# Performance work log

Measured on AMD Instinct MI355X. Metric: run time of the kernel, lower is better.

The kernel has to match this reference:

```python
import jax, jax.numpy as jnp
import numpy as np

KH = KW = 3  # kernel spatial size is hard-coded to 3 in the original layer


def _tdiv2(x):
    # matches tf.cast(x / 2, tf.int32): true-divide by 2, truncate toward zero
    return jnp.trunc(x * 0.5)


def setup_inputs() -> dict:
    key = jax.random.key(0)
    k1, k2, k3 = jax.random.split(key, 3)
    B, H, W, C, F = 4, 32, 32, 64, 128
    # integer-valued tensors stored as float32 (bit-serial math needs integer weights)
    inputs = jax.random.randint(k1, (B, H, W, C), 0, 16).astype(jnp.float32)
    kernel = jax.random.randint(k2, (KH, KW, C, F), -8, 8).astype(jnp.float32)
    bias = jax.random.randint(k3, (F,), -4, 4).astype(jnp.float32)
    return {"inputs": inputs, "kernel": kernel, "bias": bias, "bits": 4}


def reference(inputs, kernel, bias, bits):
    # Bit-serial conv2d, padding='same' (pad=1), activation='relu'.
    # Per (kernel position, input element, output channel) the original computes
    #   acc <- trunc((acc + x * (w mod 2) * sign(w_orig)) / 2); w <- trunc(w / 2)
    # for `bits` iterations, then sums over channels/kernel window.
    B, H, W, C = inputs.shape
    F = kernel.shape[-1]
    x = jnp.pad(inputs, ((0, 0), (1, 1), (1, 1), (0, 0)))  # 'same' padding, pad=1
    out = jnp.zeros((B, H, W, F), inputs.dtype)
    for i in range(KH):
        for j in range(KW):
            patch = x[:, i:i + H, j:j + W, :][..., None]   # [B,H,W,C,1]
            w = kernel[i, j]                               # [C,F]
            s = jnp.sign(w)                                # sign of ORIGINAL weight, fixed
            acc = jnp.zeros((B, H, W, C, F), inputs.dtype)
            ww = w
            for _ in range(bits):
                acc = _tdiv2(acc + patch * (jnp.mod(ww, 2.0) * s))
                ww = _tdiv2(ww)
            out = out + acc.sum(axis=3)                    # sum over C; kernel window summed by loop
    return jax.nn.relu(out + bias)
```

## Files before the change

### kernel.cpp

```cpp
#include <hip/hip_runtime.h>
#include <stdint.h>


typedef short s16x2 __attribute__((ext_vector_type(2)));

#define NWPK 36864
#define XOFF 36864
#define NXPK 147968

__global__ __launch_bounds__(256) void prep_all(const float* __restrict__ kern,
                                                const float* __restrict__ input,
                                                uint32_t* __restrict__ ws) {
    int bid = blockIdx.x, tid = threadIdx.x;
    if (bid < 144) {
        int t  = bid * 256 + tid;
        int u  = t & 3;
        int f  = (t >> 2) & 127;
        int cq = (t >> 9) & 3;
        int gk = t >> 11;
        int g  = gk & 1;
        int ki = gk >> 1;
        int c  = cq * 16 + g * 8 + u * 2;
        int wlo = (int)kern[(ki * 64 + c    ) * 128 + f];
        int whi = (int)kern[(ki * 64 + c + 1) * 128 + f];
        ws[t] = (uint32_t)(uint16_t)(int16_t)wlo |
                ((uint32_t)(uint16_t)(int16_t)whi << 16);
    } else {
        int t = (bid - 144) * 256 + tid;
        if (t >= NXPK) return;
        int c2    = t & 31;
        int rest  = t >> 5;
        int wp    = rest % 34;
        int rest2 = rest / 34;
        int hp    = rest2 % 34;
        int b     = rest2 / 34;
        int v = 0;
        if (hp >= 1 && hp <= 32 && wp >= 1 && wp <= 32) {
            const float* p = &input[(((b * 32) + hp - 1) * 32 + (wp - 1)) * 64 + c2 * 2];
            v = (int)p[0] | ((int)p[1] << 16);
        }
        ws[XOFF + t] = (uint32_t)v;
    }
}

__global__ __launch_bounds__(512, 4) void conv_main(const uint32_t* __restrict__ ws,
                                                    const float* __restrict__ bias,
                                                    float* __restrict__ out) {
    const uint32_t* xpk = ws + XOFF;

    int bid = blockIdx.x;
    int wq  = bid & 7;
    int h   = (bid >> 3) & 31;
    int b   = bid >> 8;
    int tid = threadIdx.x;
    int f   = tid & 127;
    int cq  = tid >> 7;
    int w0  = wq * 4;

    __shared__ uint32_t xl[3 * 6 * 32];
    __shared__ int prt[4 * 4 * 128];

    if (tid < 576) {
        int c2  = tid & 31;
        int rc  = tid >> 5;
        int col = rc % 6;
        int r   = rc / 6;
        xl[tid] = xpk[((b * 34 + h + r) * 34 + (w0 + col)) * 32 + c2];
    } else {
        int k   = tid - 512;
    }
    if (tid < 64) {
        int k   = tid + 512;
        int c2  = k & 31;
        int rc  = k >> 5;
        int col = rc % 6;
        int r   = rc / 6;
        xl[k] = xpk[((b * 34 + h + r) * 34 + (w0 + col)) * 32 + c2];
    }

    int4 wv[18];
    const int4* wp = (const int4*)ws;
    #pragma unroll
    for (int i = 0; i < 18; ++i) wv[i] = wp[i * 512 + tid];

    __syncthreads();

    s16x2 acc0 = {0,0}, acc1 = {0,0}, acc2 = {0,0}, acc3 = {0,0};

    #pragma unroll
    for (int ki = 0; ki < 9; ++ki) {
        const int row = ki / 3, jj = ki % 3;
        #pragma unroll
        for (int g = 0; g < 2; ++g) {
            const int4 w4 = wv[ki * 2 + g];
            const uint32_t* xrow = xl + (row * 6 + jj) * 32 + cq * 8 + g * 4;
            int4 xv0 = *(const int4*)(xrow);
            int4 xv1 = *(const int4*)(xrow + 32);
            int4 xv2 = *(const int4*)(xrow + 64);
            int4 xv3 = *(const int4*)(xrow + 96);
            #pragma unroll
            for (int u = 0; u < 4; ++u) {
                s16x2 w2 = __builtin_bit_cast(s16x2, (&w4.x)[u]);
                s16x2 A  = (w2 >> 15) & (short)15;
                acc0 += (__builtin_bit_cast(s16x2, (&xv0.x)[u]) * w2 + A) >> 4;
                acc1 += (__builtin_bit_cast(s16x2, (&xv1.x)[u]) * w2 + A) >> 4;
                acc2 += (__builtin_bit_cast(s16x2, (&xv2.x)[u]) * w2 + A) >> 4;
                acc3 += (__builtin_bit_cast(s16x2, (&xv3.x)[u]) * w2 + A) >> 4;
            }
        }
    }

    int a;
    a = __builtin_bit_cast(int, acc0); prt[(cq * 4 + 0) * 128 + f] = (int)(short)(a & 0xffff) + (a >> 16);
    a = __builtin_bit_cast(int, acc1); prt[(cq * 4 + 1) * 128 + f] = (int)(short)(a & 0xffff) + (a >> 16);
    a = __builtin_bit_cast(int, acc2); prt[(cq * 4 + 2) * 128 + f] = (int)(short)(a & 0xffff) + (a >> 16);
    a = __builtin_bit_cast(int, acc3); prt[(cq * 4 + 3) * 128 + f] = (int)(short)(a & 0xffff) + (a >> 16);
    __syncthreads();

    {
        int ff = tid & 127;
        int px = tid >> 7;
        int v = prt[(0 * 4 + px) * 128 + ff] + prt[(1 * 4 + px) * 128 + ff] +
                prt[(2 * 4 + px) * 128 + ff] + prt[(3 * 4 + px) * 128 + ff] +
                (int)bias[ff];
        out[((b * 32 + h) * 32 + w0 + px) * 128 + ff] = (float)(v < 0 ? 0 : v);
    }
}

extern "C" void kernel_launch(void* const* d_in, const int* in_sizes, int n_in,
                              void* d_out, int out_size, void* d_ws, size_t ws_size,
                              hipStream_t stream) {
    const float* input  = (const float*)d_in[0];
    const float* kernel = (const float*)d_in[1];
    const float* bias   = (const float*)d_in[2];

    uint32_t* ws = (uint32_t*)d_ws;

    prep_all<<<144 + 579, 256, 0, stream>>>(kernel, input, ws);
    conv_main<<<1024, 512, 0, stream>>>(ws, bias, (float*)d_out);
}
```

Baseline: 79.23 us.

## Fuse input packing into conv kernel and widen tile to 8 pixels

Input packing and padding move out of the prep kernel and into conv_main, which now reads float4 input directly and packs it into shared memory with bounds checks. The prep kernel only packs weights. Each conv block now covers 8 output pixels instead of 4, halving the grid and reusing each weight load across more pixels. Weights are loaded from global memory inside the loop rather than prefetched into 18 registers. Together these aim to cut the intermediate global round-trip and weight traffic, at the cost of more accumulators and in-loop load latency.

```diff
diff --git a/kernel.cpp b/kernel.cpp
--- a/kernel.cpp
+++ b/kernel.cpp
@@ -5,125 +5,104 @@
 typedef short s16x2 __attribute__((ext_vector_type(2)));
 
 #define NWPK 36864
-#define XOFF 36864
-#define NXPK 147968
 
-__global__ __launch_bounds__(256) void prep_all(const float* __restrict__ kern,
-                                                const float* __restrict__ input,
-                                                uint32_t* __restrict__ ws) {
-    int bid = blockIdx.x, tid = threadIdx.x;
-    if (bid < 144) {
-        int t  = bid * 256 + tid;
-        int u  = t & 3;
-        int f  = (t >> 2) & 127;
-        int cq = (t >> 9) & 3;
-        int gk = t >> 11;
-        int g  = gk & 1;
-        int ki = gk >> 1;
-        int c  = cq * 16 + g * 8 + u * 2;
-        int wlo = (int)kern[(ki * 64 + c    ) * 128 + f];
-        int whi = (int)kern[(ki * 64 + c + 1) * 128 + f];
-        ws[t] = (uint32_t)(uint16_t)(int16_t)wlo |
-                ((uint32_t)(uint16_t)(int16_t)whi << 16);
-    } else {
-        int t = (bid - 144) * 256 + tid;
-        if (t >= NXPK) return;
-        int c2    = t & 31;
-        int rest  = t >> 5;
-        int wp    = rest % 34;
-        int rest2 = rest / 34;
-        int hp    = rest2 % 34;
-        int b     = rest2 / 34;
-        int v = 0;
-        if (hp >= 1 && hp <= 32 && wp >= 1 && wp <= 32) {
-            const float* p = &input[(((b * 32) + hp - 1) * 32 + (wp - 1)) * 64 + c2 * 2];
-            v = (int)p[0] | ((int)p[1] << 16);
-        }
-        ws[XOFF + t] = (uint32_t)v;
-    }
+__global__ __launch_bounds__(256) void prep_w(const float* __restrict__ kern,
+                                              uint32_t* __restrict__ ws) {
+    int t  = blockIdx.x * 256 + threadIdx.x;
+    int u  = t & 3;
+    int f  = (t >> 2) & 127;
+    int cq = (t >> 9) & 3;
+    int gk = t >> 11;
+    int g  = gk & 1;
+    int ki = gk >> 1;
+    int c  = cq * 16 + g * 8 + u * 2;
+    int wlo = (int)kern[(ki * 64 + c    ) * 128 + f];
+    int whi = (int)kern[(ki * 64 + c + 1) * 128 + f];
+    ws[t] = (uint32_t)(uint16_t)(int16_t)wlo |
+            ((uint32_t)(uint16_t)(int16_t)whi << 16);
 }
 
 __global__ __launch_bounds__(512, 4) void conv_main(const uint32_t* __restrict__ ws,
+                                                    const float* __restrict__ input,
                                                     const float* __restrict__ bias,
                                                     float* __restrict__ out) {
-    const uint32_t* xpk = ws + XOFF;
-
     int bid = blockIdx.x;
-    int wq  = bid & 7;
-    int h   = (bid >> 3) & 31;
-    int b   = bid >> 8;
+    int wq  = bid & 3;
+    int h   = (bid >> 2) & 31;
+    int b   = bid >> 7;
     int tid = threadIdx.x;
     int f   = tid & 127;
     int cq  = tid >> 7;
-    int w0  = wq * 4;
+    int w0  = wq * 8;
 
-    __shared__ uint32_t xl[3 * 6 * 32];
-    __shared__ int prt[4 * 4 * 128];
+    __shared__ uint32_t xl[3 * 10 * 32];
+    __shared__ int prt[4 * 8 * 128];
 
-    if (tid < 576) {
-        int c2  = tid & 31;
-        int rc  = tid >> 5;
-        int col = rc % 6;
-        int r   = rc / 6;
-        xl[tid] = xpk[((b * 34 + h + r) * 34 + (w0 + col)) * 32 + c2];
-    } else {
-        int k   = tid - 512;
-    }
-    if (tid < 64) {
-        int k   = tid + 512;
-        int c2  = k & 31;
-        int rc  = k >> 5;
-        int col = rc % 6;
-        int r   = rc / 6;
-        xl[k] = xpk[((b * 34 + h + r) * 34 + (w0 + col)) * 32 + c2];
+    if (tid < 480) {
+        int q   = tid & 15;
+        int rc  = tid >> 4;
+        int col = rc % 10;
+        int r   = rc / 10;
+        int hp  = h + r - 1;
+        int wp  = w0 + col - 1;
+        int2 v2 = {0, 0};
+        if (hp >= 0 && hp < 32 && wp >= 0 && wp < 32) {
+            const float4 v = *(const float4*)&input[(((b * 32) + hp) * 32 + wp) * 64 + q * 4];
+            v2.x = (int)v.x | ((int)v.y << 16);
+            v2.y = (int)v.z | ((int)v.w << 16);
+        }
+        *(int2*)&xl[rc * 32 + q * 2] = v2;
     }
 
-    int4 wv[18];
-    const int4* wp = (const int4*)ws;
-    #pragma unroll
-    for (int i = 0; i < 18; ++i) wv[i] = wp[i * 512 + tid];
+    const int4* wp4 = (const int4*)ws;
+    int bv = (int)bias[f];
 
     __syncthreads();
 
-    s16x2 acc0 = {0,0}, acc1 = {0,0}, acc2 = {0,0}, acc3 = {0,0};
+    s16x2 acc[8];
+    #pragma unroll
+    for (int i = 0; i < 8; ++i) acc[i] = (s16x2){0, 0};
 
     #pragma unroll
     for (int ki = 0; ki < 9; ++ki) {
         const int row = ki / 3, jj = ki % 3;
         #pragma unroll
         for (int g = 0; g < 2; ++g) {
-            const int4 w4 = wv[ki * 2 + g];
-            const uint32_t* xrow = xl + (row * 6 + jj) * 32 + cq * 8 + g * 4;
-            int4 xv0 = *(const int4*)(xrow);
-            int4 xv1 = *(const int4*)(xrow + 32);
-            int4 xv2 = *(const int4*)(xrow + 64);
-            int4 xv3 = *(const int4*)(xrow + 96);
+            const int4 w4 = wp4[(ki * 2 + g) * 512 + tid];
+            const uint32_t* xrow = xl + (row * 10 + jj) * 32 + cq * 8 + g * 4;
             #pragma unroll
-            for (int u = 0; u < 4; ++u) {
-                s16x2 w2 = __builtin_bit_cast(s16x2, (&w4.x)[u]);
-                s16x2 A  = (w2 >> 15) & (short)15;
-                acc0 += (__builtin_bit_cast(s16x2, (&xv0.x)[u]) * w2 + A) >> 4;
-                acc1 += (__builtin_bit_cast(s16x2, (&xv1.x)[u]) * w2 + A) >> 4;
-                acc2 += (__builtin_bit_cast(s16x2, (&xv2.x)[u]) * w2 + A) >> 4;
-                acc3 += (__builtin_bit_cast(s16x2, (&xv3.x)[u]) * w2 + A) >> 4;
+            for (int half = 0; half < 2; ++half) {
+                int4 xv[4];
+                #pragma unroll
+                for (int p = 0; p < 4; ++p)
+                    xv[p] = *(const int4*)(xrow + (half * 4 + p) * 32);
+                #pragma unroll
+                for (int u = 0; u < 4; ++u) {
+                    s16x2 w2 = __builtin_bit_cast(s16x2, (&w4.x)[u]);
+                    s16x2 A  = (w2 >> 15) & (short)15;
+                    #pragma unroll
+                    for (int p = 0; p < 4; ++p) {
+                        s16x2 xs = __builtin_bit_cast(s16x2, (&xv[p].x)[u]);
+                        acc[half * 4 + p] += (xs * w2 + A) >> 4;
+                    }
+                }
             }
         }
     }
 
-    int a;
-    a = __builtin_bit_cast(int, acc0); prt[(cq * 4 + 0) * 128 + f] = (int)(short)(a & 0xffff) + (a >> 16);
-    a = __builtin_bit_cast(int, acc1); prt[(cq * 4 + 1) * 128 + f] = (int)(short)(a & 0xffff) + (a >> 16);
-    a = __builtin_bit_cast(int, acc2); prt[(cq * 4 + 2) * 128 + f] = (int)(short)(a & 0xffff) + (a >> 16);
-    a = __builtin_bit_cast(int, acc3); prt[(cq * 4 + 3) * 128 + f] = (int)(short)(a & 0xffff) + (a >> 16);
+    #pragma unroll
+    for (int px = 0; px < 8; ++px) {
+        int a = __builtin_bit_cast(int, acc[px]);
+        prt[(cq * 8 + px) * 128 + f] = (int)(short)(a & 0xffff) + (a >> 16);
+    }
     __syncthreads();
 
-    {
-        int ff = tid & 127;
-        int px = tid >> 7;
-        int v = prt[(0 * 4 + px) * 128 + ff] + prt[(1 * 4 + px) * 128 + ff] +
-                prt[(2 * 4 + px) * 128 + ff] + prt[(3 * 4 + px) * 128 + ff] +
-                (int)bias[ff];
-        out[((b * 32 + h) * 32 + w0 + px) * 128 + ff] = (float)(v < 0 ? 0 : v);
+    #pragma unroll
+    for (int k = 0; k < 2; ++k) {
+        int px = (tid >> 7) + k * 4;
+        int v = prt[(0 * 8 + px) * 128 + f] + prt[(1 * 8 + px) * 128 + f] +
+                prt[(2 * 8 + px) * 128 + f] + prt[(3 * 8 + px) * 128 + f] + bv;
+        out[((b * 32 + h) * 32 + w0 + px) * 128 + f] = (float)(v < 0 ? 0 : v);
     }
 }
 
@@ -136,6 +115,6 @@
 
     uint32_t* ws = (uint32_t*)d_ws;
 
-    prep_all<<<144 + 579, 256, 0, stream>>>(kernel, input, ws);
-    conv_main<<<1024, 512, 0, stream>>>(ws, bias, (float*)d_out);
+    prep_w<<<144, 256, 0, stream>>>(kernel, ws);
+    conv_main<<<512, 512, 0, stream>>>(ws, input, bias, (float*)d_out);
 }
```

Measured after the change: 76.83 us. -3.0%, faster.
